# Kernel tuning notes

Hardware: AMD Instinct MI355X
Metric: run time of the kernel (lower is better)

Reference implementation:

```python
import jax, jax.numpy as jnp
from jax import lax
import numpy as np

B, H, W = 8, 512, 512
HW = H * W  # sentinel label for non-mask pixels


def _label_components(mask):
    """4-connectivity connected-component labeling (min flat-index per component).
    mask: [H,W] bool. Returns [HW] int32 labels; non-mask pixels get label HW.
    Label propagation + pointer jumping -> O(log diameter) iterations."""
    idx = jnp.arange(HW, dtype=jnp.int32).reshape(H, W)
    lab0 = jnp.where(mask, idx, HW)

    def step(lab):
        p = jnp.pad(lab, 1, mode='constant', constant_values=HW)
        nb = jnp.minimum(jnp.minimum(p[:-2, 1:-1], p[2:, 1:-1]),
                         jnp.minimum(p[1:-1, :-2], p[1:-1, 2:]))
        new = jnp.where(mask, jnp.minimum(lab, nb), HW)
        flat = new.reshape(-1)
        flat_ext = jnp.concatenate([flat, jnp.array([HW], dtype=flat.dtype)])
        new = jnp.minimum(flat, flat_ext[flat]).reshape(H, W)  # pointer jump
        return jnp.where(mask, new, HW)

    def cond(state):
        return state[1]

    def body(state):
        lab, _ = state
        new = step(lab)
        return new, jnp.any(new != lab)

    lab, _ = lax.while_loop(cond, body, (lab0, jnp.array(True)))
    return lab.reshape(-1)


def _keep_large(mask):
    """Keep pixels belonging to components with area > max_area/2 (matches
    ndi.label + ndi.sum + thresholded relabel; ndi.sum scaling by 255/1 cancels)."""
    labels = _label_components(mask)  # [HW]
    counts = jax.ops.segment_sum(mask.reshape(-1).astype(jnp.float32), labels,
                                 num_segments=HW + 1)  # counts[HW]=0 (non-mask contributes 0)
    max_area = counts.max()
    keep = mask.reshape(-1) & (counts[labels] > 0.5 * max_area)
    return keep.reshape(mask.shape)


def _masked_ce(logits, target):
    """CrossEntropyLoss(ignore_index=255, reduction='mean'). logits [B,C,H,W], target [B,H,W]."""
    logp = jax.nn.log_softmax(logits, axis=1)
    valid = target != 255
    tc = jnp.where(valid, target, 0)
    nll = -jnp.take_along_axis(logp, tc[:, None], axis=1)[:, 0]  # [B,H,W]
    denom = jnp.maximum(jnp.sum(valid), 1).astype(logp.dtype)
    return jnp.sum(jnp.where(valid, nll, 0.0)) / denom


def setup_inputs() -> dict:
    key = jax.random.key(0)
    k1, k2 = jax.random.split(key)
    preds = jax.random.normal(k1, (3, B, 2, H, W), dtype=jnp.float32)
    cams = jax.random.uniform(k2, (B, 1, H, W), dtype=jnp.float32)
    return {"preds": preds, "cams": cams}


def reference(preds, cams):
    cam = cams[:, 0]                      # [B,H,W]
    bg_mask = cam >= 0.2                  # pixels left at 255 in bg_label (the labeled regions)
    fg_mask = cam > 0.6                   # pixels set to 1 in fg_label
    keep_bg = jax.vmap(_keep_large)(bg_mask)
    keep_fg = jax.vmap(_keep_large)(fg_mask)
    bg_t = jnp.where(keep_bg, 255, 0).astype(jnp.int32)   # large uncertain regions ignored
    fg_t = jnp.where(keep_fg, 1, 255).astype(jnp.int32)   # small/non-fg ignored
    loss = jnp.float32(0.0)
    for i in range(preds.shape[0]):       # weight (1**i / 1) == 1
        loss = loss + _masked_ce(preds[i], fg_t) + _masked_ce(preds[i], bg_t)
    return loss
```

## Files before the change

### kernel.cpp

```cpp
#include <hip/hip_runtime.h>
#include <hip/hip_bf16.h>
#include <math.h>

#define Bsz    8
#define Wdim   512
#define HWv    (512 * 512)
#define LOG2HW 18
#define NIMG   16
#define TILE   64
#define TPIX   (TILE * TILE)


__device__ __forceinline__ int uf_find(int* L, int x) {
  int p = L[x];
  while (p != x) {
    int gp = L[p];
    if (gp != p) atomicMin(&L[x], gp);
    x = gp;
    p = L[x];
  }
  return x;
}

__device__ __forceinline__ int find_ro(const int* __restrict__ L, int x) {
  int p = L[x];
  while (p != x) { x = p; p = L[x]; }
  return x;
}

__device__ __forceinline__ void uf_union(int* L, int a, int b) {
  a = uf_find(L, a);
  b = uf_find(L, b);
  while (a != b) {
    if (a < b) { int t = a; a = b; b = t; }
    int old = atomicMin(&L[a], b);
    if (old == a) return;
    a = old;
  }
}


__global__ __launch_bounds__(1024) void k_local(const float* __restrict__ cams,
                                                int* __restrict__ labels,
                                                int* __restrict__ areas) {
  int img  = blockIdx.x >> 6;
  int tile = blockIdx.x & 63;
  int tY = tile >> 3, tX = tile & 7;
  int b = img & 7;
  bool fg = (img & 8) != 0;
  int gbase = img << LOG2HW;
  int oy = tY * TILE, ox = tX * TILE;
  int lane = threadIdx.x & 63;

  __shared__ int P[TPIX];
  __shared__ int A[TPIX];

  #pragma unroll
  for (int it = 0; it < 4; ++it) {
    int i  = it * 1024 + threadIdx.x;
    int ly = i >> 6;
    float c = cams[(b << LOG2HW) + ((oy + ly) << 9) + (ox + lane)];
    bool m = fg ? (c > 0.6f) : (c >= 0.2f);
    unsigned long long bm = __ballot(m);
    int par = -1;
    if (m) {
      unsigned long long below = (1ULL << lane) - 1ULL;
      unsigned long long z = (~bm) & below;
      int rs = z ? (64 - __clzll(z)) : 0;
      par = (ly << 6) + rs;
    }
    P[i] = par;
    A[i] = 0;
  }
  __syncthreads();

  #pragma unroll
  for (int it = 0; it < 4; ++it) {
    int i = it * 1024 + threadIdx.x;
    if (i >= TILE && P[i] >= 0 && P[i - TILE] >= 0) {
      bool skip = (lane > 0) && (P[i - 1] >= 0) && (P[i - TILE - 1] >= 0);
      if (!skip) uf_union(P, i, i - TILE);
    }
  }
  __syncthreads();

  #pragma unroll
  for (int it = 0; it < 4; ++it) {
    int i = it * 1024 + threadIdx.x;
    bool m = P[i] >= 0;
    unsigned long long bm = __ballot(m);
    int rs = 0;
    if (m) {
      unsigned long long below = (1ULL << lane) - 1ULL;
      unsigned long long z = (~bm) & below;
      rs = z ? (64 - __clzll(z)) : 0;
    }
    bool isStart = m && (rs == lane);
    int r = -1;
    if (isStart) r = find_ro(P, i);
    int root = __shfl(r, rs);
    if (m) P[i] = root;
    if (isStart) {
      unsigned long long t = (~bm) >> lane;
      int runlen = t ? (__ffsll((long long)t) - 1) : (64 - lane);
      atomicAdd(&A[root], runlen);
    }
  }
  __syncthreads();

  #pragma unroll
  for (int it = 0; it < 4; ++it) {
    int i  = it * 1024 + threadIdx.x;
    int ly = i >> 6;
    int g  = ((oy + ly) << 9) + (ox + lane);
    int p  = P[i];
    int lab = -1;
    if (p >= 0) lab = ((oy + (p >> 6)) << 9) + (ox + (p & 63));
    labels[gbase + g] = lab;
    areas[gbase + g]  = (p == i) ? A[i] : 0;
  }
}

__global__ void k_border(int* __restrict__ labels, int* __restrict__ maxa,
                         double* __restrict__ sums, int* __restrict__ counts) {
  if (blockIdx.x == 0) {
    if (threadIdx.x < NIMG) maxa[threadIdx.x] = 0;
    if (threadIdx.x < 2) { sums[threadIdx.x] = 0.0; counts[threadIdx.x] = 0; }
  }
  const int per_img = 14 * Wdim;
  int t = blockIdx.x * blockDim.x + threadIdx.x;
  if (t >= NIMG * per_img) return;
  int img = t / per_img;
  int r   = t - img * per_img;
  int k = r >> 9, j = r & (Wdim - 1);
  int* L = labels + (img << LOG2HW);
  if (k < 7) {
    int x = TILE * k + (TILE - 1);
    int p = (j << 9) + x, q = p + 1;
    if (L[p] >= 0 && L[q] >= 0) {
      bool skip = (j > 0) && (L[p - Wdim] >= 0) && (L[q - Wdim] >= 0);
      if (!skip) uf_union(L, p, q);
    }
  } else {
    int y = TILE * (k - 7) + (TILE - 1);
    int p = (y << 9) + j, q = p + Wdim;
    if (L[p] >= 0 && L[q] >= 0) {
      bool skip = (j > 0) && (L[p - 1] >= 0) && (L[q - 1] >= 0);
      if (!skip) uf_union(L, p, q);
    }
  }
}

__global__ void k_flatten(int* __restrict__ labels, int* __restrict__ areas) {
  int t = blockIdx.x * blockDim.x + threadIdx.x;
  int idx0 = t << 2;
  int4 ar = *(const int4*)&areas[idx0];
  if ((ar.x | ar.y | ar.z | ar.w) <= 0) return;
  int img  = idx0 >> LOG2HW;
  int base = img << LOG2HW;
  int* L = labels + base;
  int self0 = idx0 - base;
  int4 lab = *(const int4*)&labels[idx0];
  if (ar.x > 0) { int r = find_ro(L, lab.x); L[self0]     = r; if (r != self0)     atomicAdd(&areas[base + r], ar.x); }
  if (ar.y > 0) { int r = find_ro(L, lab.y); L[self0 + 1] = r; if (r != self0 + 1) atomicAdd(&areas[base + r], ar.y); }
  if (ar.z > 0) { int r = find_ro(L, lab.z); L[self0 + 2] = r; if (r != self0 + 2) atomicAdd(&areas[base + r], ar.z); }
  if (ar.w > 0) { int r = find_ro(L, lab.w); L[self0 + 3] = r; if (r != self0 + 3) atomicAdd(&areas[base + r], ar.w); }
}

__global__ void k_max(const int* __restrict__ areas, int* __restrict__ maxa) {
  int img = blockIdx.x >> 4;
  int seg = blockIdx.x & 15;
  const int4* a4 = (const int4*)(areas + (img << LOG2HW));
  int base = seg * (HWv / 4 / 16);
  int m = 0;
  #pragma unroll
  for (int k = 0; k < 16; ++k) {
    int4 v = a4[base + k * 256 + threadIdx.x];
    m = max(m, max(max(v.x, v.y), max(v.z, v.w)));
  }
  #pragma unroll
  for (int off = 32; off > 0; off >>= 1)
    m = max(m, __shfl_down(m, off));
  __shared__ int lm[4];
  int wave = threadIdx.x >> 6;
  if ((threadIdx.x & 63) == 0) lm[wave] = m;
  __syncthreads();
  if (threadIdx.x == 0) {
    int bm = max(max(lm[0], lm[1]), max(lm[2], lm[3]));
    if (bm > 0) atomicMax(&maxa[img], bm);
  }
}

__global__ __launch_bounds__(1024) void k_keepce(const float* __restrict__ preds,
                                                 const int* __restrict__ labels,
                                                 const int* __restrict__ areas,
                                                 const int* __restrict__ maxa,
                                                 double* __restrict__ sums,
                                                 int* __restrict__ counts) {
  int b    = blockIdx.x >> 6;
  int tile = blockIdx.x & 63;
  int tY = tile >> 3, tX = tile & 7;
  int oy = tY * TILE, ox = tX * TILE;
  int basebg = b << LOG2HW, basefg = (8 + b) << LOG2HW;
  int maxb = maxa[b], maxf = maxa[8 + b];

  __shared__ int Vbg[TPIX];
  __shared__ int Vfg[TPIX];

  int i  = threadIdx.x << 2;
  int ly = i >> 6, lx = i & 63;
  int g  = ((oy + ly) << 9) + (ox + lx);
  int4 lb = *(const int4*)&labels[basebg + g];
  int4 lf = *(const int4*)&labels[basefg + g];
  int4 ab = *(const int4*)&areas[basebg + g];
  int4 af = *(const int4*)&areas[basefg + g];
  if (ab.x > 0) { Vbg[i+0] = (2 * areas[basebg + lb.x] > maxb); lb.x = g + 0; }
  if (ab.y > 0) { Vbg[i+1] = (2 * areas[basebg + lb.y] > maxb); lb.y = g + 1; }
  if (ab.z > 0) { Vbg[i+2] = (2 * areas[basebg + lb.z] > maxb); lb.z = g + 2; }
  if (ab.w > 0) { Vbg[i+3] = (2 * areas[basebg + lb.w] > maxb); lb.w = g + 3; }
  if (af.x > 0) { Vfg[i+0] = (2 * areas[basefg + lf.x] > maxf); lf.x = g + 0; }
  if (af.y > 0) { Vfg[i+1] = (2 * areas[basefg + lf.y] > maxf); lf.y = g + 1; }
  if (af.z > 0) { Vfg[i+2] = (2 * areas[basefg + lf.z] > maxf); lf.z = g + 2; }
  if (af.w > 0) { Vfg[i+3] = (2 * areas[basefg + lf.w] > maxf); lf.w = g + 3; }
  __syncthreads();

  float4 A0[3], A1[3];
  #pragma unroll
  for (int p = 0; p < 3; p++) {
    const float* pb = preds + ((size_t)((p * Bsz + b) * 2) << LOG2HW);
    A0[p] = *(const float4*)&pb[g];
    A1[p] = *(const float4*)&pb[HWv + g];
  }
  int lbj[4] = {lb.x, lb.y, lb.z, lb.w};
  int lfj[4] = {lf.x, lf.y, lf.z, lf.w};
  bool vf[4], vb[4];
  #pragma unroll
  for (int j = 0; j < 4; j++) {
    int locb = (((lbj[j] >> 9) & 63) << 6) | (lbj[j] & 63);
    int locf = (((lfj[j] >> 9) & 63) << 6) | (lfj[j] & 63);
    bool kb = (lbj[j] >= 0) && (Vbg[locb] != 0);
    bool kf = (lfj[j] >= 0) && (Vfg[locf] != 0);
    vb[j] = !kb;
    vf[j] = kf;
  }
  int cf = (int)vf[0] + vf[1] + vf[2] + vf[3];
  int cb = (int)vb[0] + vb[1] + vb[2] + vb[3];
  float sfg = 0.f, sbg = 0.f;
  #pragma unroll
  for (int p = 0; p < 3; p++) {
    float d[4] = {A0[p].x - A1[p].x, A0[p].y - A1[p].y,
                  A0[p].z - A1[p].z, A0[p].w - A1[p].w};
    #pragma unroll
    for (int j = 0; j < 4; j++) {
      float sp = logf(1.f + expf(-fabsf(d[j])));
      sfg += vf[j] ? (fmaxf(d[j], 0.f) + sp) : 0.f;
      sbg += vb[j] ? (fmaxf(-d[j], 0.f) + sp) : 0.f;
    }
  }
  #pragma unroll
  for (int off = 32; off > 0; off >>= 1) {
    sfg += __shfl_down(sfg, off);
    sbg += __shfl_down(sbg, off);
    cf  += __shfl_down(cf, off);
    cb  += __shfl_down(cb, off);
  }
  __shared__ float lsf[16], lsb[16];
  __shared__ int   lcf[16], lcb[16];
  int wave = threadIdx.x >> 6;
  if ((threadIdx.x & 63) == 0) {
    lsf[wave] = sfg; lsb[wave] = sbg; lcf[wave] = cf; lcb[wave] = cb;
  }
  __syncthreads();
  if (threadIdx.x == 0) {
    float tf = 0.f, tb = 0.f; int af_ = 0, ab_ = 0;
    #pragma unroll
    for (int w = 0; w < 16; w++) { tf += lsf[w]; tb += lsb[w]; af_ += lcf[w]; ab_ += lcb[w]; }
    atomicAdd(&sums[0], (double)tf);
    atomicAdd(&sums[1], (double)tb);
    atomicAdd(&counts[0], af_);
    atomicAdd(&counts[1], ab_);
  }
}

__global__ void k_final(const double* __restrict__ sums, const int* __restrict__ counts,
                        float* __restrict__ out) {
  if (threadIdx.x == 0 && blockIdx.x == 0) {
    double df = counts[0] > 0 ? (double)counts[0] : 1.0;
    double db = counts[1] > 0 ? (double)counts[1] : 1.0;
    out[0] = (float)(sums[0] / df + sums[1] / db);
  }
}

extern "C" void kernel_launch(void* const* d_in, const int* in_sizes, int n_in,
                              void* d_out, int out_size, void* d_ws, size_t ws_size,
                              hipStream_t stream) {
  (void)in_sizes; (void)n_in; (void)out_size; (void)ws_size;
  const float* preds = (const float*)d_in[0];
  const float* cams  = (const float*)d_in[1];
  float* out = (float*)d_out;

  int* labels = (int*)d_ws;
  int* areas  = labels + NIMG * HWv;
  int* maxa   = areas + NIMG * HWv;
  double* sums = (double*)(maxa + 16);
  int* counts  = (int*)(sums + 2);

  const int threads = 256;

  k_local  <<<NIMG * 64, 1024, 0, stream>>>(cams, labels, areas);
  k_border <<<(NIMG * 14 * Wdim + threads - 1) / threads, threads, 0, stream>>>(labels, maxa, sums, counts);
  k_flatten<<<NIMG * HWv / (threads * 4), threads, 0, stream>>>(labels, areas);
  k_max    <<<NIMG * 16, threads, 0, stream>>>(areas, maxa);
  k_keepce <<<Bsz * 64, 1024, 0, stream>>>(preds, labels, areas, maxa, sums, counts);
  k_final  <<<1, 64, 0, stream>>>(sums, counts, out);
}
```

Measured before the change: 166.6 us.

## Compact per-tile root lists and 16-bit local labels to avoid full-image scans

The local labeling kernel now handles both masks in one block, sharing a single cams load. It writes 16-bit tile-local labels, a compact per-tile list of root pixels packed with their areas, and tile-edge label arrays. The border, flatten and max kernels now walk only the edge arrays and root lists instead of scanning full label and area images. The keep/CE kernel builds its keep table from the root lists and reads 16-bit labels. The aim is to cut global memory traffic and dead threads, at the cost of more workspace buffers and a fixed per-tile root capacity (RCAP 2048), which a 64x64 tile with 4-connectivity cannot exceed.

```diff
diff --git a/kernel.cpp b/kernel.cpp
--- a/kernel.cpp
+++ b/kernel.cpp
@@ -9,6 +9,7 @@
 #define NIMG   16
 #define TILE   64
 #define TPIX   (TILE * TILE)
+#define RCAP   2048
 
 
 __device__ __forceinline__ int uf_find(int* L, int x) {
@@ -41,142 +42,184 @@
 
 
 __global__ __launch_bounds__(1024) void k_local(const float* __restrict__ cams,
-                                                int* __restrict__ labels,
-                                                int* __restrict__ areas) {
-  int img  = blockIdx.x >> 6;
+    int* __restrict__ parent, int* __restrict__ areas,
+    unsigned short* __restrict__ L16, unsigned int* __restrict__ rootPack,
+    int* __restrict__ rootCnt, int* __restrict__ bL, int* __restrict__ bR,
+    int* __restrict__ bT, int* __restrict__ bB) {
+  int b    = blockIdx.x >> 6;
   int tile = blockIdx.x & 63;
-  int tY = tile >> 3, tX = tile & 7;
-  int b = img & 7;
-  bool fg = (img & 8) != 0;
-  int gbase = img << LOG2HW;
-  int oy = tY * TILE, ox = tX * TILE;
-  int lane = threadIdx.x & 63;
-
-  __shared__ int P[TPIX];
-  __shared__ int A[TPIX];
+  int oy = (tile >> 3) * TILE, ox = (tile & 7) * TILE;
+  int tid = threadIdx.x, lane = tid & 63;
+
+  __shared__ int P[2][TPIX];
+  __shared__ int A[2][TPIX];
+  __shared__ int rc[2];
+  if (tid < 2) rc[tid] = 0;
 
   #pragma unroll
   for (int it = 0; it < 4; ++it) {
-    int i  = it * 1024 + threadIdx.x;
+    int i  = it * 1024 + tid;
     int ly = i >> 6;
-    float c = cams[(b << LOG2HW) + ((oy + ly) << 9) + (ox + lane)];
-    bool m = fg ? (c > 0.6f) : (c >= 0.2f);
-    unsigned long long bm = __ballot(m);
-    int par = -1;
-    if (m) {
-      unsigned long long below = (1ULL << lane) - 1ULL;
-      unsigned long long z = (~bm) & below;
-      int rs = z ? (64 - __clzll(z)) : 0;
-      par = (ly << 6) + rs;
-    }
-    P[i] = par;
-    A[i] = 0;
+    float c = cams[(b << LOG2HW) + ((oy + ly) << 9) + ox + lane];
+    #pragma unroll
+    for (int m = 0; m < 2; ++m) {
+      bool msk = m ? (c > 0.6f) : (c >= 0.2f);
+      unsigned long long bm = __ballot(msk);
+      int par = -1;
+      if (msk) {
+        unsigned long long below = (1ULL << lane) - 1ULL;
+        unsigned long long z = (~bm) & below;
+        int rs = z ? (64 - __clzll(z)) : 0;
+        par = (ly << 6) + rs;
+      }
+      P[m][i] = par;
+      A[m][i] = 0;
+    }
   }
   __syncthreads();
 
   #pragma unroll
   for (int it = 0; it < 4; ++it) {
-    int i = it * 1024 + threadIdx.x;
-    if (i >= TILE && P[i] >= 0 && P[i - TILE] >= 0) {
-      bool skip = (lane > 0) && (P[i - 1] >= 0) && (P[i - TILE - 1] >= 0);
-      if (!skip) uf_union(P, i, i - TILE);
+    int i = it * 1024 + tid;
+    if (i >= TILE) {
+      #pragma unroll
+      for (int m = 0; m < 2; ++m) {
+        if (P[m][i] >= 0 && P[m][i - TILE] >= 0) {
+          bool skip = (lane > 0) && (P[m][i - 1] >= 0) && (P[m][i - TILE - 1] >= 0);
+          if (!skip) uf_union(P[m], i, i - TILE);
+        }
+      }
     }
   }
   __syncthreads();
 
   #pragma unroll
   for (int it = 0; it < 4; ++it) {
-    int i = it * 1024 + threadIdx.x;
-    bool m = P[i] >= 0;
-    unsigned long long bm = __ballot(m);
-    int rs = 0;
-    if (m) {
-      unsigned long long below = (1ULL << lane) - 1ULL;
-      unsigned long long z = (~bm) & below;
-      rs = z ? (64 - __clzll(z)) : 0;
-    }
-    bool isStart = m && (rs == lane);
-    int r = -1;
-    if (isStart) r = find_ro(P, i);
-    int root = __shfl(r, rs);
-    if (m) P[i] = root;
-    if (isStart) {
-      unsigned long long t = (~bm) >> lane;
-      int runlen = t ? (__ffsll((long long)t) - 1) : (64 - lane);
-      atomicAdd(&A[root], runlen);
+    int i = it * 1024 + tid;
+    #pragma unroll
+    for (int m = 0; m < 2; ++m) {
+      bool msk = P[m][i] >= 0;
+      unsigned long long bm = __ballot(msk);
+      int rs = 0;
+      if (msk) {
+        unsigned long long below = (1ULL << lane) - 1ULL;
+        unsigned long long z = (~bm) & below;
+        rs = z ? (64 - __clzll(z)) : 0;
+      }
+      bool isStart = msk && (rs == lane);
+      int r = -1;
+      if (isStart) r = find_ro(P[m], i);
+      int root = __shfl(r, rs);
+      if (msk) P[m][i] = root;
+      if (isStart) {
+        unsigned long long t = (~bm) >> lane;
+        int runlen = t ? (__ffsll((long long)t) - 1) : (64 - lane);
+        atomicAdd(&A[m][root], runlen);
+      }
     }
   }
   __syncthreads();
 
   #pragma unroll
   for (int it = 0; it < 4; ++it) {
-    int i  = it * 1024 + threadIdx.x;
-    int ly = i >> 6;
-    int g  = ((oy + ly) << 9) + (ox + lane);
-    int p  = P[i];
-    int lab = -1;
-    if (p >= 0) lab = ((oy + (p >> 6)) << 9) + (ox + (p & 63));
-    labels[gbase + g] = lab;
-    areas[gbase + g]  = (p == i) ? A[i] : 0;
-  }
-}
-
-__global__ void k_border(int* __restrict__ labels, int* __restrict__ maxa,
+    int i  = it * 1024 + tid;
+    int ly = i >> 6, lx = i & 63;
+    int g  = ((oy + ly) << 9) + ox + lx;
+    #pragma unroll
+    for (int m = 0; m < 2; ++m) {
+      int imgm = m * 8 + b;
+      int p = P[m][i];
+      L16[((size_t)imgm << LOG2HW) + g] = (p < 0) ? (unsigned short)0xFFFF
+                                                  : (unsigned short)p;
+      if (p == i) {
+        int slot = atomicAdd(&rc[m], 1);
+        parent[(imgm << LOG2HW) + g] = g;
+        areas [(imgm << LOG2HW) + g] = 0;
+        rootPack[(((imgm << 6) + tile) * RCAP) + slot] =
+            ((unsigned)i << 13) | (unsigned)A[m][i];
+      }
+    }
+  }
+  __syncthreads();
+  if (tid < 2) rootCnt[(((tid * 8 + b) << 6) + tile)] = rc[tid];
+  if (tid < 512) {
+    int m = tid >> 8, rem = tid & 255, e = rem >> 6, k = rem & 63;
+    int i = (e == 0) ? (k << 6) : (e == 1) ? ((k << 6) + 63)
+          : (e == 2) ? k : ((63 << 6) + k);
+    int p = P[m][i];
+    int val = (p < 0) ? -1 : (((oy + (p >> 6)) << 9) + ox + (p & 63));
+    int idx = (((m * 8 + b) << 6) + tile) * 64 + k;
+    if (e == 0) bL[idx] = val; else if (e == 1) bR[idx] = val;
+    else if (e == 2) bT[idx] = val; else bB[idx] = val;
+  }
+}
+
+__global__ void k_border(int* __restrict__ parent, const int* __restrict__ bL,
+                         const int* __restrict__ bR, const int* __restrict__ bT,
+                         const int* __restrict__ bB, int* __restrict__ maxa,
                          double* __restrict__ sums, int* __restrict__ counts) {
   if (blockIdx.x == 0) {
     if (threadIdx.x < NIMG) maxa[threadIdx.x] = 0;
     if (threadIdx.x < 2) { sums[threadIdx.x] = 0.0; counts[threadIdx.x] = 0; }
   }
-  const int per_img = 14 * Wdim;
   int t = blockIdx.x * blockDim.x + threadIdx.x;
-  if (t >= NIMG * per_img) return;
-  int img = t / per_img;
-  int r   = t - img * per_img;
-  int k = r >> 9, j = r & (Wdim - 1);
-  int* L = labels + (img << LOG2HW);
-  if (k < 7) {
-    int x = TILE * k + (TILE - 1);
-    int p = (j << 9) + x, q = p + 1;
-    if (L[p] >= 0 && L[q] >= 0) {
-      bool skip = (j > 0) && (L[p - Wdim] >= 0) && (L[q - Wdim] >= 0);
-      if (!skip) uf_union(L, p, q);
+  int img = t / 7168;
+  int r   = t - img * 7168;
+  int* Lp = parent + (img << LOG2HW);
+  if (r < 3584) {
+    int v = r >> 6, y = r & 63;
+    int tXl = v >> 3, tYv = v & 7;
+    int tileL = tYv * 8 + tXl;
+    int baseR = ((img << 6) + tileL) * 64;
+    int baseL = ((img << 6) + tileL + 1) * 64;
+    int pr = bR[baseR + y], qr = bL[baseL + y];
+    if (pr >= 0 && qr >= 0) {
+      bool skip = (y > 0) && (bR[baseR + y - 1] >= 0) && (bL[baseL + y - 1] >= 0);
+      if (!skip) uf_union(Lp, pr, qr);
     }
   } else {
-    int y = TILE * (k - 7) + (TILE - 1);
-    int p = (y << 9) + j, q = p + Wdim;
-    if (L[p] >= 0 && L[q] >= 0) {
-      bool skip = (j > 0) && (L[p - 1] >= 0) && (L[q - 1] >= 0);
-      if (!skip) uf_union(L, p, q);
-    }
-  }
-}
-
-__global__ void k_flatten(int* __restrict__ labels, int* __restrict__ areas) {
-  int t = blockIdx.x * blockDim.x + threadIdx.x;
-  int idx0 = t << 2;
-  int4 ar = *(const int4*)&areas[idx0];
-  if ((ar.x | ar.y | ar.z | ar.w) <= 0) return;
-  int img  = idx0 >> LOG2HW;
-  int base = img << LOG2HW;
-  int* L = labels + base;
-  int self0 = idx0 - base;
-  int4 lab = *(const int4*)&labels[idx0];
-  if (ar.x > 0) { int r = find_ro(L, lab.x); L[self0]     = r; if (r != self0)     atomicAdd(&areas[base + r], ar.x); }
-  if (ar.y > 0) { int r = find_ro(L, lab.y); L[self0 + 1] = r; if (r != self0 + 1) atomicAdd(&areas[base + r], ar.y); }
-  if (ar.z > 0) { int r = find_ro(L, lab.z); L[self0 + 2] = r; if (r != self0 + 2) atomicAdd(&areas[base + r], ar.z); }
-  if (ar.w > 0) { int r = find_ro(L, lab.w); L[self0 + 3] = r; if (r != self0 + 3) atomicAdd(&areas[base + r], ar.w); }
-}
-
-__global__ void k_max(const int* __restrict__ areas, int* __restrict__ maxa) {
-  int img = blockIdx.x >> 4;
-  int seg = blockIdx.x & 15;
-  const int4* a4 = (const int4*)(areas + (img << LOG2HW));
-  int base = seg * (HWv / 4 / 16);
+    int r2 = r - 3584;
+    int h = r2 >> 6, x = r2 & 63;
+    int tYt = h >> 3, tX = h & 7;
+    int tileT = tYt * 8 + tX;
+    int baseB = ((img << 6) + tileT) * 64;
+    int baseT = ((img << 6) + tileT + 8) * 64;
+    int pr = bB[baseB + x], qr = bT[baseT + x];
+    if (pr >= 0 && qr >= 0) {
+      bool skip = (x > 0) && (bB[baseB + x - 1] >= 0) && (bT[baseT + x - 1] >= 0);
+      if (!skip) uf_union(Lp, pr, qr);
+    }
+  }
+}
+
+__global__ void k_flatten(int* __restrict__ parent, int* __restrict__ areas,
+                          const unsigned int* __restrict__ rootPack,
+                          int* __restrict__ rootF, const int* __restrict__ rootCnt) {
+  int lt = blockIdx.x;
+  int imgm = lt >> 6, tile = lt & 63;
+  int oy = (tile >> 3) * TILE, ox = (tile & 7) * TILE;
+  int cnt = rootCnt[lt];
+  const int* Lp = parent + (imgm << LOG2HW);
+  for (int k = threadIdx.x; k < cnt; k += blockDim.x) {
+    unsigned pk = rootPack[lt * RCAP + k];
+    int loc = pk >> 13, area = pk & 8191;
+    int gr = ((oy + (loc >> 6)) << 9) + ox + (loc & 63);
+    int f = find_ro(Lp, gr);
+    atomicAdd(&areas[(imgm << LOG2HW) + f], area);
+    rootF[lt * RCAP + k] = f;
+  }
+}
+
+__global__ void k_max(const int* __restrict__ areas, int* __restrict__ rootF,
+                      const int* __restrict__ rootCnt, int* __restrict__ maxa) {
+  int lt = blockIdx.x;
+  int imgm = lt >> 6;
+  int cnt = rootCnt[lt];
   int m = 0;
-  #pragma unroll
-  for (int k = 0; k < 16; ++k) {
-    int4 v = a4[base + k * 256 + threadIdx.x];
-    m = max(m, max(max(v.x, v.y), max(v.z, v.w)));
+  for (int k = threadIdx.x; k < cnt; k += blockDim.x) {
+    int tot = areas[(imgm << LOG2HW) + rootF[lt * RCAP + k]];
+    rootF[lt * RCAP + k] = tot;
+    m = max(m, tot);
   }
   #pragma unroll
   for (int off = 32; off > 0; off >>= 1)
@@ -187,43 +230,36 @@
   __syncthreads();
   if (threadIdx.x == 0) {
     int bm = max(max(lm[0], lm[1]), max(lm[2], lm[3]));
-    if (bm > 0) atomicMax(&maxa[img], bm);
+    if (bm > 0) atomicMax(&maxa[imgm], bm);
   }
 }
 
 __global__ __launch_bounds__(1024) void k_keepce(const float* __restrict__ preds,
-                                                 const int* __restrict__ labels,
-                                                 const int* __restrict__ areas,
-                                                 const int* __restrict__ maxa,
-                                                 double* __restrict__ sums,
-                                                 int* __restrict__ counts) {
-  int b    = blockIdx.x >> 6;
-  int tile = blockIdx.x & 63;
-  int tY = tile >> 3, tX = tile & 7;
-  int oy = tY * TILE, ox = tX * TILE;
-  int basebg = b << LOG2HW, basefg = (8 + b) << LOG2HW;
-  int maxb = maxa[b], maxf = maxa[8 + b];
-
-  __shared__ int Vbg[TPIX];
-  __shared__ int Vfg[TPIX];
-
-  int i  = threadIdx.x << 2;
-  int ly = i >> 6, lx = i & 63;
-  int g  = ((oy + ly) << 9) + (ox + lx);
-  int4 lb = *(const int4*)&labels[basebg + g];
-  int4 lf = *(const int4*)&labels[basefg + g];
-  int4 ab = *(const int4*)&areas[basebg + g];
-  int4 af = *(const int4*)&areas[basefg + g];
-  if (ab.x > 0) { Vbg[i+0] = (2 * areas[basebg + lb.x] > maxb); lb.x = g + 0; }
-  if (ab.y > 0) { Vbg[i+1] = (2 * areas[basebg + lb.y] > maxb); lb.y = g + 1; }
-  if (ab.z > 0) { Vbg[i+2] = (2 * areas[basebg + lb.z] > maxb); lb.z = g + 2; }
-  if (ab.w > 0) { Vbg[i+3] = (2 * areas[basebg + lb.w] > maxb); lb.w = g + 3; }
-  if (af.x > 0) { Vfg[i+0] = (2 * areas[basefg + lf.x] > maxf); lf.x = g + 0; }
-  if (af.y > 0) { Vfg[i+1] = (2 * areas[basefg + lf.y] > maxf); lf.y = g + 1; }
-  if (af.z > 0) { Vfg[i+2] = (2 * areas[basefg + lf.z] > maxf); lf.z = g + 2; }
-  if (af.w > 0) { Vfg[i+3] = (2 * areas[basefg + lf.w] > maxf); lf.w = g + 3; }
-  __syncthreads();
-
+    const unsigned short* __restrict__ L16, const unsigned int* __restrict__ rootPack,
+    const int* __restrict__ rootF, const int* __restrict__ rootCnt,
+    const int* __restrict__ maxa, double* __restrict__ sums, int* __restrict__ counts) {
+  int b = blockIdx.x >> 6, tile = blockIdx.x & 63;
+  int oy = (tile >> 3) * TILE, ox = (tile & 7) * TILE;
+  __shared__ unsigned short V[2][TPIX];
+  int mx0 = maxa[b], mx1 = maxa[8 + b];
+  #pragma unroll
+  for (int m = 0; m < 2; ++m) {
+    int lt = (((m * 8 + b) << 6) + tile);
+    int cnt = rootCnt[lt];
+    int mxm = m ? mx1 : mx0;
+    for (int k = threadIdx.x; k < cnt; k += 1024) {
+      unsigned pk = rootPack[lt * RCAP + k];
+      int tot = rootF[lt * RCAP + k];
+      V[m][pk >> 13] = (2 * tot > mxm) ? 1 : 0;
+    }
+  }
+  __syncthreads();
+
+  int i0 = threadIdx.x << 2;
+  int ly = i0 >> 6, lx = i0 & 63;
+  int g  = ((oy + ly) << 9) + ox + lx;
+  ushort4 ub4 = *(const ushort4*)&L16[((size_t)b << LOG2HW) + g];
+  ushort4 uf4 = *(const ushort4*)&L16[((size_t)(8 + b) << LOG2HW) + g];
   float4 A0[3], A1[3];
   #pragma unroll
   for (int p = 0; p < 3; p++) {
@@ -231,15 +267,13 @@
     A0[p] = *(const float4*)&pb[g];
     A1[p] = *(const float4*)&pb[HWv + g];
   }
-  int lbj[4] = {lb.x, lb.y, lb.z, lb.w};
-  int lfj[4] = {lf.x, lf.y, lf.z, lf.w};
+  unsigned short lb[4] = {ub4.x, ub4.y, ub4.z, ub4.w};
+  unsigned short lf[4] = {uf4.x, uf4.y, uf4.z, uf4.w};
   bool vf[4], vb[4];
   #pragma unroll
   for (int j = 0; j < 4; j++) {
-    int locb = (((lbj[j] >> 9) & 63) << 6) | (lbj[j] & 63);
-    int locf = (((lfj[j] >> 9) & 63) << 6) | (lfj[j] & 63);
-    bool kb = (lbj[j] >= 0) && (Vbg[locb] != 0);
-    bool kf = (lfj[j] >= 0) && (Vfg[locf] != 0);
+    bool kb = (lb[j] != 0xFFFF) && (V[0][lb[j] & 4095] != 0);
+    bool kf = (lf[j] != 0xFFFF) && (V[1][lf[j] & 4095] != 0);
     vb[j] = !kb;
     vf[j] = kf;
   }
@@ -299,18 +333,27 @@
   const float* cams  = (const float*)d_in[1];
   float* out = (float*)d_out;
 
-  int* labels = (int*)d_ws;
-  int* areas  = labels + NIMG * HWv;
-  int* maxa   = areas + NIMG * HWv;
+  int* parent = (int*)d_ws;
+  int* areas  = parent + (NIMG << LOG2HW);
+  unsigned short* L16 = (unsigned short*)(areas + (NIMG << LOG2HW));
+  unsigned int* rootPack = (unsigned int*)(L16 + ((size_t)NIMG << LOG2HW));
+  int* rootF   = (int*)(rootPack + NIMG * 64 * RCAP);
+  int* rootCnt = rootF + NIMG * 64 * RCAP;
+  int* bL = rootCnt + NIMG * 64;
+  int* bR = bL + NIMG * 64 * 64;
+  int* bT = bR + NIMG * 64 * 64;
+  int* bB = bT + NIMG * 64 * 64;
+  int* maxa = bB + NIMG * 64 * 64;
   double* sums = (double*)(maxa + 16);
   int* counts  = (int*)(sums + 2);
 
-  const int threads = 256;
-
-  k_local  <<<NIMG * 64, 1024, 0, stream>>>(cams, labels, areas);
-  k_border <<<(NIMG * 14 * Wdim + threads - 1) / threads, threads, 0, stream>>>(labels, maxa, sums, counts);
-  k_flatten<<<NIMG * HWv / (threads * 4), threads, 0, stream>>>(labels, areas);
-  k_max    <<<NIMG * 16, threads, 0, stream>>>(areas, maxa);
-  k_keepce <<<Bsz * 64, 1024, 0, stream>>>(preds, labels, areas, maxa, sums, counts);
+  k_local  <<<Bsz * 64, 1024, 0, stream>>>(cams, parent, areas, L16, rootPack,
+                                           rootCnt, bL, bR, bT, bB);
+  k_border <<<NIMG * 7168 / 256, 256, 0, stream>>>(parent, bL, bR, bT, bB,
+                                                   maxa, sums, counts);
+  k_flatten<<<NIMG * 64, 256, 0, stream>>>(parent, areas, rootPack, rootF, rootCnt);
+  k_max    <<<NIMG * 64, 256, 0, stream>>>(areas, rootF, rootCnt, maxa);
+  k_keepce <<<Bsz * 64, 1024, 0, stream>>>(preds, L16, rootPack, rootF, rootCnt,
+                                           maxa, sums, counts);
   k_final  <<<1, 64, 0, stream>>>(sums, counts, out);
 }
```

After: 168.5 us. About the same (+1.1%).
